# Kernel tuning notes

Hardware: AMD Instinct MI355X
Metric: run time of the kernel (lower is better)

## Reference

```python
import jax, jax.numpy as jnp
import numpy as np

N = 100000
E = 3200000
C = 32

def setup_inputs() -> dict:
    key = jax.random.key(0)
    k1, k2, k3, k4 = jax.random.split(key, 4)
    adj = jax.random.uniform(k1, (E,), dtype=jnp.float32)          # per-edge weights
    labels = jax.random.uniform(k2, (N, C), dtype=jnp.float32)     # node label distributions
    src = jax.random.randint(k3, (E,), 0, N, dtype=jnp.int64)
    dst = jax.random.randint(k4, (E,), 0, N, dtype=jnp.int64)
    return {"adj": adj, "labels": labels, "src": src, "dst": dst, "n_lpa": 3}

def reference(adj, labels, src, dst, n_lpa):
    # One hop of label propagation: msg_e = label[src_e] * w_e; out_v = sum_{e: dst_e=v} msg_e
    n_nodes = labels.shape[0]

    def lp(lab):
        msg = lab[src] * adj[:, None]                 # [E, C] gather-multiply
        return jax.ops.segment_sum(msg, dst, num_segments=n_nodes)  # scatter-sum over dst

    # soft_label == 0 path of the original forward: plain iterated propagation
    for _ in range(n_lpa):
        labels = lp(labels)
    return labels
```

## Files before the change

### kernel.cpp

```cpp
#include <hip/hip_runtime.h>


#define LPA_C   32
#define BKT_LG  7
#define BKT_NV  (1 << BKT_LG)
#define CHUNK   12800

__global__ __launch_bounds__(1024)
void k_histA(const int* __restrict__ dst, int* __restrict__ C,
             int E, int P, int nbkt) {
    __shared__ int h[1024];
    int c = blockIdx.x;
    int base = c * CHUNK;
    int lim = min(CHUNK, E - base);
    for (int i = threadIdx.x; i < nbkt; i += 1024) h[i] = 0;
    __syncthreads();
    for (int i = threadIdx.x; i < lim; i += 1024)
        atomicAdd(&h[dst[base + i] >> BKT_LG], 1);
    __syncthreads();
    for (int i = threadIdx.x; i < nbkt; i += 1024) C[i * P + c] = h[i];
}

__global__ void k_scanC(int* __restrict__ C, int* __restrict__ btot, int P) {
    __shared__ int s[256];
    int b = blockIdx.x;
    int t = threadIdx.x;
    int v = (t < P) ? C[b * P + t] : 0;
    s[t] = v;
    __syncthreads();
    for (int off = 1; off < 256; off <<= 1) {
        int x = (t >= off) ? s[t - off] : 0;
        __syncthreads();
        s[t] += x;
        __syncthreads();
    }
    if (t < P) C[b * P + t] = s[t] - v;
    if (t == 255) btot[b] = s[255];
}

__global__ __launch_bounds__(1024)
void k_scanB(const int* __restrict__ btot, int* __restrict__ bstart,
             int* __restrict__ row_start, int nb, int N, int E) {
    __shared__ int s[1024];
    int t = threadIdx.x;
    int v = (t < nb) ? btot[t] : 0;
    s[t] = v;
    __syncthreads();
    for (int off = 1; off < 1024; off <<= 1) {
        int x = (t >= off) ? s[t - off] : 0;
        __syncthreads();
        s[t] += x;
        __syncthreads();
    }
    if (t < nb) bstart[t] = s[t] - v;
    if (t == 0) { bstart[nb] = E; row_start[N] = E; }
}

__global__ __launch_bounds__(1024)
void k_scatA(const int* __restrict__ src, const int* __restrict__ dst,
             const float* __restrict__ adj, const int* __restrict__ C,
             const int* __restrict__ bstart, int2* __restrict__ mid,
             int E, int P, int nbkt) {
    __shared__ int cur[1024];
    int c = blockIdx.x;
    int base = c * CHUNK;
    int lim = min(CHUNK, E - base);
    for (int i = threadIdx.x; i < nbkt; i += 1024)
        cur[i] = bstart[i] + C[i * P + c];
    __syncthreads();
    for (int i = threadIdx.x; i < lim; i += 1024) {
        int d = dst[base + i];
        int b = d >> BKT_LG;
        int pos = atomicAdd(&cur[b], 1);
        mid[pos] = make_int2(src[base + i] | ((d & (BKT_NV - 1)) << 20),
                             __float_as_int(adj[base + i]));
    }
}

__global__ __launch_bounds__(512)
void k_sortnode(const int2* __restrict__ mid, const int* __restrict__ bstart,
                int2* __restrict__ edges, int* __restrict__ row_start, int N) {
    __shared__ int lcnt[BKT_NV];
    __shared__ int lofs[BKT_NV];
    int b = blockIdx.x;
    int s0 = bstart[b], e0 = bstart[b + 1];
    int v0 = b << BKT_LG;
    int nv = min(BKT_NV, N - v0);

    if (threadIdx.x < BKT_NV) lcnt[threadIdx.x] = 0;
    __syncthreads();
    for (int i = s0 + threadIdx.x; i < e0; i += 512)
        atomicAdd(&lcnt[mid[i].x >> 20], 1);
    __syncthreads();
    if (threadIdx.x < BKT_NV) lofs[threadIdx.x] = lcnt[threadIdx.x];
    __syncthreads();
    for (int off = 1; off < BKT_NV; off <<= 1) {
        int x = 0;
        if (threadIdx.x < BKT_NV && threadIdx.x >= off) x = lofs[threadIdx.x - off];
        __syncthreads();
        if (threadIdx.x < BKT_NV) lofs[threadIdx.x] += x;
        __syncthreads();
    }
    if (threadIdx.x < BKT_NV) {
        int base = s0 + lofs[threadIdx.x] - lcnt[threadIdx.x];
        lcnt[threadIdx.x] = base;
        if (threadIdx.x < nv) row_start[v0 + threadIdx.x] = base;
    }
    __syncthreads();
    for (int i = s0 + threadIdx.x; i < e0; i += 512) {
        int2 ed = mid[i];
        int pos = atomicAdd(&lcnt[ed.x >> 20], 1);
        edges[pos] = make_int2(ed.x & 0xFFFFF, ed.y);
    }
}

__global__ void lpa_pull(const int2* __restrict__ edges,
                         const int* __restrict__ row_start,
                         const float* __restrict__ lab_in,
                         float* __restrict__ out, int N) {
    int node = blockIdx.x * 8 + (threadIdx.x >> 5);
    int c = threadIdx.x & 31;
    if (node >= N) return;
    int j = row_start[node];
    int end = row_start[node + 1];
    float acc0 = 0.f, acc1 = 0.f;
    for (; j + 8 <= end; j += 8) {
        int2 e0 = edges[j],     e1 = edges[j + 1], e2 = edges[j + 2], e3 = edges[j + 3];
        int2 e4 = edges[j + 4], e5 = edges[j + 5], e6 = edges[j + 6], e7 = edges[j + 7];
        acc0 += __int_as_float(e0.y) * lab_in[((size_t)e0.x << 5) + c];
        acc1 += __int_as_float(e1.y) * lab_in[((size_t)e1.x << 5) + c];
        acc0 += __int_as_float(e2.y) * lab_in[((size_t)e2.x << 5) + c];
        acc1 += __int_as_float(e3.y) * lab_in[((size_t)e3.x << 5) + c];
        acc0 += __int_as_float(e4.y) * lab_in[((size_t)e4.x << 5) + c];
        acc1 += __int_as_float(e5.y) * lab_in[((size_t)e5.x << 5) + c];
        acc0 += __int_as_float(e6.y) * lab_in[((size_t)e6.x << 5) + c];
        acc1 += __int_as_float(e7.y) * lab_in[((size_t)e7.x << 5) + c];
    }
    for (; j < end; ++j) {
        int2 e = edges[j];
        acc0 += __int_as_float(e.y) * lab_in[((size_t)e.x << 5) + c];
    }
    out[((size_t)node << 5) + c] = acc0 + acc1;
}

__global__ void lpa_scatter_fb(const float* __restrict__ adj,
                               const float* __restrict__ lab_in,
                               const int* __restrict__ src,
                               const int* __restrict__ dst,
                               float* __restrict__ out, int E) {
    long long idx = (long long)blockIdx.x * blockDim.x + threadIdx.x;
    int e = (int)(idx >> 5);
    if (e >= E) return;
    int c = (int)(idx & 31);
    float v = lab_in[(long long)src[e] * LPA_C + c] * adj[e];
    unsafeAtomicAdd(&out[(long long)dst[e] * LPA_C + c], v);
}

extern "C" void kernel_launch(void* const* d_in, const int* in_sizes, int n_in,
                              void* d_out, int out_size, void* d_ws, size_t ws_size,
                              hipStream_t stream) {
    const float* adj    = (const float*)d_in[0];
    const float* labels = (const float*)d_in[1];
    const int*   src    = (const int*)d_in[2];
    const int*   dst    = (const int*)d_in[3];

    const int E  = in_sizes[0];
    const int NC = in_sizes[1];
    const int N  = NC / LPA_C;
    const int NBKT = (N + BKT_NV - 1) >> BKT_LG;
    const int P  = (E + CHUNK - 1) / CHUNK;
    float* out = (float*)d_out;

    char* p = (char*)d_ws;
    int2*  edges     = (int2*)p;  p += (size_t)E * sizeof(int2);
    int2*  mid       = (int2*)p;  p += (size_t)E * sizeof(int2);
    int*   C         = (int*)p;   p += (size_t)NBKT * P * sizeof(int);
    int*   btot      = (int*)p;   p += (size_t)NBKT * sizeof(int);
    int*   bstart    = (int*)p;   p += (size_t)(NBKT + 1) * sizeof(int);
    int*   row_start = (int*)p;   p += (size_t)(N + 1) * sizeof(int);
    size_t needed = (size_t)(p - (char*)d_ws);
    float* ws_lab = (float*)mid;

    if (ws_size < needed || NBKT > 1024 || P > 256 || N >= (1 << 20)) {
        float* ws0 = (float*)d_ws;
        const size_t nbytes = (size_t)NC * sizeof(float);
        const long long total = (long long)E * LPA_C;
        const unsigned grid = (unsigned)((total + 255) / 256);
        hipMemsetAsync(out, 0, nbytes, stream);
        lpa_scatter_fb<<<grid, 256, 0, stream>>>(adj, labels, src, dst, out, E);
        hipMemsetAsync(ws0, 0, nbytes, stream);
        lpa_scatter_fb<<<grid, 256, 0, stream>>>(adj, out, src, dst, ws0, E);
        hipMemsetAsync(out, 0, nbytes, stream);
        lpa_scatter_fb<<<grid, 256, 0, stream>>>(adj, ws0, src, dst, out, E);
        return;
    }

    k_histA   <<<P, 1024, 0, stream>>>(dst, C, E, P, NBKT);
    k_scanC   <<<NBKT, 256, 0, stream>>>(C, btot, P);
    k_scanB   <<<1, 1024, 0, stream>>>(btot, bstart, row_start, NBKT, N, E);
    k_scatA   <<<P, 1024, 0, stream>>>(src, dst, adj, C, bstart, mid, E, P, NBKT);
    k_sortnode<<<NBKT, 512, 0, stream>>>(mid, bstart, edges, row_start, N);

    const unsigned gridN = (unsigned)((N + 7) / 8);
    lpa_pull<<<gridN, 256, 0, stream>>>(edges, row_start, labels, out, N);
    lpa_pull<<<gridN, 256, 0, stream>>>(edges, row_start, out, ws_lab, N);
    lpa_pull<<<gridN, 256, 0, stream>>>(edges, row_start, ws_lab, out, N);
}
```

Before: 256.9 us.

## Sort each node's edges by source window and split pull across half-waves

The per-bucket node sort now keys on (local dst, src>>13), so each node's edge list is grouped into coarse source windows. Across the wavefront this should give the label gathers better L2 locality. The pull kernel now gives each node a full 64-lane wave, with the two half-waves handling alternating edges and combined by a cross-lane shuffle. This adds more independent loads in flight but halves the number of nodes per block. The fallback guard now caps N at 16<<13, and the sort kernel carries a larger shared counter array and a 512-wide scan.

Result: slower. 308.6 us (+20.1%).

```diff
diff --git a/kernel.cpp b/kernel.cpp
--- a/kernel.cpp
+++ b/kernel.cpp
@@ -5,6 +5,9 @@
 #define BKT_LG  7
 #define BKT_NV  (1 << BKT_LG)
 #define CHUNK   12800
+#define WIN_LG  13
+#define MAXW    16
+#define NKEY    (BKT_NV * MAXW)
 
 __global__ __launch_bounds__(1024)
 void k_histA(const int* __restrict__ dst, int* __restrict__ C,
@@ -80,37 +83,50 @@
 __global__ __launch_bounds__(512)
 void k_sortnode(const int2* __restrict__ mid, const int* __restrict__ bstart,
                 int2* __restrict__ edges, int* __restrict__ row_start, int N) {
-    __shared__ int lcnt[BKT_NV];
-    __shared__ int lofs[BKT_NV];
+    __shared__ int kcnt[NKEY];
+    __shared__ int s2[512];
     int b = blockIdx.x;
     int s0 = bstart[b], e0 = bstart[b + 1];
     int v0 = b << BKT_LG;
     int nv = min(BKT_NV, N - v0);
-
-    if (threadIdx.x < BKT_NV) lcnt[threadIdx.x] = 0;
-    __syncthreads();
-    for (int i = s0 + threadIdx.x; i < e0; i += 512)
-        atomicAdd(&lcnt[mid[i].x >> 20], 1);
-    __syncthreads();
-    if (threadIdx.x < BKT_NV) lofs[threadIdx.x] = lcnt[threadIdx.x];
-    __syncthreads();
-    for (int off = 1; off < BKT_NV; off <<= 1) {
-        int x = 0;
-        if (threadIdx.x < BKT_NV && threadIdx.x >= off) x = lofs[threadIdx.x - off];
-        __syncthreads();
-        if (threadIdx.x < BKT_NV) lofs[threadIdx.x] += x;
-        __syncthreads();
-    }
-    if (threadIdx.x < BKT_NV) {
-        int base = s0 + lofs[threadIdx.x] - lcnt[threadIdx.x];
-        lcnt[threadIdx.x] = base;
-        if (threadIdx.x < nv) row_start[v0 + threadIdx.x] = base;
-    }
-    __syncthreads();
-    for (int i = s0 + threadIdx.x; i < e0; i += 512) {
+    int t = threadIdx.x;
+
+    for (int i = t; i < NKEY; i += 512) kcnt[i] = 0;
+    __syncthreads();
+    for (int i = s0 + t; i < e0; i += 512) {
         int2 ed = mid[i];
-        int pos = atomicAdd(&lcnt[ed.x >> 20], 1);
-        edges[pos] = make_int2(ed.x & 0xFFFFF, ed.y);
+        int key = ((ed.x >> 20) << 4) | ((ed.x & 0xFFFFF) >> WIN_LG);
+        atomicAdd(&kcnt[key], 1);
+    }
+    __syncthreads();
+
+    int base = t * 4;
+    int a0 = kcnt[base], a1 = kcnt[base + 1], a2 = kcnt[base + 2], a3 = kcnt[base + 3];
+    int tsum = a0 + a1 + a2 + a3;
+    s2[t] = tsum;
+    __syncthreads();
+    for (int off = 1; off < 512; off <<= 1) {
+        int x = (t >= off) ? s2[t - off] : 0;
+        __syncthreads();
+        s2[t] += x;
+        __syncthreads();
+    }
+    int pre = s2[t] - tsum;
+    kcnt[base]     = pre;
+    kcnt[base + 1] = pre + a0;
+    kcnt[base + 2] = pre + a0 + a1;
+    kcnt[base + 3] = pre + a0 + a1 + a2;
+    __syncthreads();
+
+    if (t < nv) row_start[v0 + t] = s0 + kcnt[t << 4];
+    __syncthreads();
+
+    for (int i = s0 + t; i < e0; i += 512) {
+        int2 ed = mid[i];
+        int srcv = ed.x & 0xFFFFF;
+        int key = ((ed.x >> 20) << 4) | (srcv >> WIN_LG);
+        int pos = s0 + atomicAdd(&kcnt[key], 1);
+        edges[pos] = make_int2(srcv, ed.y);
     }
 }
 
@@ -118,29 +134,32 @@
                          const int* __restrict__ row_start,
                          const float* __restrict__ lab_in,
                          float* __restrict__ out, int N) {
-    int node = blockIdx.x * 8 + (threadIdx.x >> 5);
-    int c = threadIdx.x & 31;
+    int node = blockIdx.x * 4 + (threadIdx.x >> 6);
     if (node >= N) return;
-    int j = row_start[node];
-    int end = row_start[node + 1];
-    float acc0 = 0.f, acc1 = 0.f;
-    for (; j + 8 <= end; j += 8) {
-        int2 e0 = edges[j],     e1 = edges[j + 1], e2 = edges[j + 2], e3 = edges[j + 3];
-        int2 e4 = edges[j + 4], e5 = edges[j + 5], e6 = edges[j + 6], e7 = edges[j + 7];
-        acc0 += __int_as_float(e0.y) * lab_in[((size_t)e0.x << 5) + c];
-        acc1 += __int_as_float(e1.y) * lab_in[((size_t)e1.x << 5) + c];
-        acc0 += __int_as_float(e2.y) * lab_in[((size_t)e2.x << 5) + c];
-        acc1 += __int_as_float(e3.y) * lab_in[((size_t)e3.x << 5) + c];
-        acc0 += __int_as_float(e4.y) * lab_in[((size_t)e4.x << 5) + c];
-        acc1 += __int_as_float(e5.y) * lab_in[((size_t)e5.x << 5) + c];
-        acc0 += __int_as_float(e6.y) * lab_in[((size_t)e6.x << 5) + c];
-        acc1 += __int_as_float(e7.y) * lab_in[((size_t)e7.x << 5) + c];
-    }
-    for (; j < end; ++j) {
-        int2 e = edges[j];
-        acc0 += __int_as_float(e.y) * lab_in[((size_t)e.x << 5) + c];
-    }
-    out[((size_t)node << 5) + c] = acc0 + acc1;
+    int lane = threadIdx.x & 63;
+    int half = lane >> 5;
+    int c = lane & 31;
+    int s = row_start[node];
+    int e = row_start[node + 1];
+    float a0 = 0.f, a1 = 0.f, a2 = 0.f, a3 = 0.f;
+    int jb = s;
+    for (; jb + 8 <= e; jb += 8) {
+        int2 e0 = edges[jb + half];
+        int2 e1 = edges[jb + 2 + half];
+        int2 e2 = edges[jb + 4 + half];
+        int2 e3 = edges[jb + 6 + half];
+        a0 += __int_as_float(e0.y) * lab_in[((size_t)e0.x << 5) + c];
+        a1 += __int_as_float(e1.y) * lab_in[((size_t)e1.x << 5) + c];
+        a2 += __int_as_float(e2.y) * lab_in[((size_t)e2.x << 5) + c];
+        a3 += __int_as_float(e3.y) * lab_in[((size_t)e3.x << 5) + c];
+    }
+    for (int j = jb + half; j < e; j += 2) {
+        int2 ee = edges[j];
+        a0 += __int_as_float(ee.y) * lab_in[((size_t)ee.x << 5) + c];
+    }
+    float acc = (a0 + a1) + (a2 + a3);
+    acc += __shfl_xor(acc, 32);
+    if (half == 0) out[((size_t)node << 5) + c] = acc;
 }
 
 __global__ void lpa_scatter_fb(const float* __restrict__ adj,
@@ -181,7 +200,7 @@
     size_t needed = (size_t)(p - (char*)d_ws);
     float* ws_lab = (float*)mid;
 
-    if (ws_size < needed || NBKT > 1024 || P > 256 || N >= (1 << 20)) {
+    if (ws_size < needed || NBKT > 1024 || P > 256 || N > (MAXW << WIN_LG)) {
         float* ws0 = (float*)d_ws;
         const size_t nbytes = (size_t)NC * sizeof(float);
         const long long total = (long long)E * LPA_C;
@@ -201,7 +220,7 @@
     k_scatA   <<<P, 1024, 0, stream>>>(src, dst, adj, C, bstart, mid, E, P, NBKT);
     k_sortnode<<<NBKT, 512, 0, stream>>>(mid, bstart, edges, row_start, N);
 
-    const unsigned gridN = (unsigned)((N + 7) / 8);
+    const unsigned gridN = (unsigned)((N + 3) / 4);
     lpa_pull<<<gridN, 256, 0, stream>>>(edges, row_start, labels, out, N);
     lpa_pull<<<gridN, 256, 0, stream>>>(edges, row_start, out, ws_lab, N);
     lpa_pull<<<gridN, 256, 0, stream>>>(edges, row_start, ws_lab, out, N);
```
